# Kernel optimization log

Measured on AMD Instinct MI355X. Metric: run time of the kernel, lower is better.

The kernel has to match this reference:

```python
import jax, jax.numpy as jnp
import numpy as np

DETER, STOCH, ACT, HID, OBS = 1024, 32, 6, 1024, 1024
B, T = 256, 64

def _lin(x, w, b):
    return x @ w.T + b

def setup_inputs() -> dict:
    key = jax.random.key(0)
    ks = iter(jax.random.split(key, 40))
    def p(shape, scale=0.02):
        return (jax.random.normal(next(ks), shape, dtype=jnp.float32) * scale)
    inp = {
        "obs": jax.random.normal(next(ks), (B, T, OBS), dtype=jnp.float32),
        "actions": jax.random.normal(next(ks), (B, T, ACT), dtype=jnp.float32),
        "eps_prior": jax.random.normal(next(ks), (B, T, STOCH), dtype=jnp.float32),
        "eps_post": jax.random.normal(next(ks), (B, T, STOCH), dtype=jnp.float32),
        # input_mlp
        "in_w1": p((HID, STOCH + ACT)), "in_b1": p((HID,)),
        "in_w2": p((HID, HID)), "in_b2": p((HID,)),
        # GRUCell (torch layout: r,z,n chunks)
        "gru_wih": p((3 * DETER, HID)), "gru_whh": p((3 * DETER, DETER)),
        "gru_bih": p((3 * DETER,)), "gru_bhh": p((3 * DETER,)),
        # prior
        "pr_w1": p((HID, DETER)), "pr_b1": p((HID,)),
        "pr_w2": p((HID, HID)), "pr_b2": p((HID,)),
        "pr_mw": p((STOCH, HID)), "pr_mb": p((STOCH,)),
        "pr_sw": p((STOCH, HID)), "pr_sb": p((STOCH,)),
        # posterior
        "po_w1": p((HID, DETER + OBS)), "po_b1": p((HID,)),
        "po_w2": p((HID, HID)), "po_b2": p((HID,)),
        "po_mw": p((STOCH, HID)), "po_mb": p((STOCH,)),
        "po_sw": p((STOCH, HID)), "po_sb": p((STOCH,)),
    }
    return inp

def _rollout(obs, actions, eps_prior, eps_post,
             in_w1, in_b1, in_w2, in_b2,
             gru_wih, gru_whh, gru_bih, gru_bhh,
             pr_w1, pr_b1, pr_w2, pr_b2, pr_mw, pr_mb, pr_sw, pr_sb,
             po_w1, po_b1, po_w2, po_b2, po_mw, po_mb, po_sw, po_sb):
    Bn = obs.shape[0]
    h0 = jnp.zeros((Bn, DETER), obs.dtype)
    z0 = jnp.zeros((Bn, STOCH), obs.dtype)
    a0 = jnp.zeros((Bn, ACT), obs.dtype)

    def step(carry, xs):
        h, z, prev_a = carry
        obs_t, act_t, ep, eq = xs
        x = jnp.concatenate([z, prev_a], axis=-1)
        x = jax.nn.relu(_lin(x, in_w1, in_b1))
        x = jax.nn.relu(_lin(x, in_w2, in_b2))
        # GRUCell
        gi = _lin(x, gru_wih, gru_bih)
        gh = _lin(h, gru_whh, gru_bhh)
        ir, iz, inn = jnp.split(gi, 3, axis=-1)
        hr, hz, hn = jnp.split(gh, 3, axis=-1)
        r = jax.nn.sigmoid(ir + hr)
        u = jax.nn.sigmoid(iz + hz)
        n = jnp.tanh(inn + r * hn)
        h_new = (1.0 - u) * n + u * h
        # prior
        px = jax.nn.relu(_lin(h_new, pr_w1, pr_b1))
        px = jax.nn.relu(_lin(px, pr_w2, pr_b2))
        p_mean = _lin(px, pr_mw, pr_mb)
        p_std = jnp.exp(jnp.clip(_lin(px, pr_sw, pr_sb), -5.0, 2.0))
        # posterior
        qx = jnp.concatenate([h_new, obs_t], axis=-1)
        qx = jax.nn.relu(_lin(qx, po_w1, po_b1))
        qx = jax.nn.relu(_lin(qx, po_w2, po_b2))
        q_mean = _lin(qx, po_mw, po_mb)
        q_std = jnp.exp(jnp.clip(_lin(qx, po_sw, po_sb), -5.0, 2.0))
        z_new = q_mean + q_std * eq
        feat = jnp.concatenate([h_new, z_new], axis=-1)
        return (h_new, z_new, act_t), (feat, p_mean, p_std, q_mean, q_std)

    xs = (jnp.swapaxes(obs, 0, 1), jnp.swapaxes(actions, 0, 1),
          jnp.swapaxes(eps_prior, 0, 1), jnp.swapaxes(eps_post, 0, 1))
    _, (feat, pm, ps, qm, qs) = jax.lax.scan(step, (h0, z0, a0), xs)
    to_bt = lambda a: jnp.swapaxes(a, 0, 1)  # [T,B,...] -> [B,T,...]
    return to_bt(feat), to_bt(pm), to_bt(ps), to_bt(qm), to_bt(qs)

def reference(obs, actions, eps_prior, eps_post,
              in_w1, in_b1, in_w2, in_b2,
              gru_wih, gru_whh, gru_bih, gru_bhh,
              pr_w1, pr_b1, pr_w2, pr_b2, pr_mw, pr_mb, pr_sw, pr_sb,
              po_w1, po_b1, po_w2, po_b2, po_mw, po_mb, po_sw, po_sb):
    return _rollout(obs, actions, eps_prior, eps_post,
                    in_w1, in_b1, in_w2, in_b2,
                    gru_wih, gru_whh, gru_bih, gru_bhh,
                    pr_w1, pr_b1, pr_w2, pr_b2, pr_mw, pr_mb, pr_sw, pr_sb,
                    po_w1, po_b1, po_w2, po_b2, po_mw, po_mb, po_sw, po_sb)
```

## Files before the change

### kernel.cpp

```cpp
#include <hip/hip_runtime.h>
#include <hip/hip_bf16.h>

#define B_   256
#define T_   64
#define OBS_ 1024
#define ACT_ 6
#define STO_ 32
#define HID_ 1024

using bf16 = __bf16;
typedef __attribute__((ext_vector_type(8))) __bf16 bf16x8;
typedef __attribute__((ext_vector_type(4))) float f32x4;

__device__ __forceinline__ f32x4 MF(bf16x8 a, bf16x8 b, f32x4 c) {
  return __builtin_amdgcn_mfma_f32_16x16x32_bf16(a, b, c, 0, 0, 0);
}

struct CvtArgs {
  const float *in_w2, *gru_wih, *gru_whh, *pr_w1, *pr_w2, *po_w1, *po_w2;
  const float *pr_mw, *pr_sw, *po_mw, *po_sw, *obs;
  bf16 *w_in2b, *w_wihb, *w_whhb, *w_pr1b, *w_pr2b, *w_po1hb, *w_po1ob, *w_po2b, *w_headb, *obsb;
};

__global__ void k_cvtall(CvtArgs a) {
  const int row = blockIdx.x;
  const float* src; bf16* dst;
  if      (row < 1024)  { src = a.in_w2   + (size_t)row * 1024;               dst = a.w_in2b  + (size_t)row * 1024; }
  else if (row < 4096)  { int r = row - 1024;  src = a.gru_wih + (size_t)r * 1024;        dst = a.w_wihb  + (size_t)r * 1024; }
  else if (row < 7168)  { int r = row - 4096;  src = a.gru_whh + (size_t)r * 1024;        dst = a.w_whhb  + (size_t)r * 1024; }
  else if (row < 8192)  { int r = row - 7168;  src = a.pr_w1   + (size_t)r * 1024;        dst = a.w_pr1b  + (size_t)r * 1024; }
  else if (row < 9216)  { int r = row - 8192;  src = a.pr_w2   + (size_t)r * 1024;        dst = a.w_pr2b  + (size_t)r * 1024; }
  else if (row < 10240) { int r = row - 9216;  src = a.po_w1   + (size_t)r * 2048;        dst = a.w_po1hb + (size_t)r * 1024; }
  else if (row < 11264) { int r = row - 10240; src = a.po_w1   + (size_t)r * 2048 + 1024; dst = a.w_po1ob + (size_t)r * 1024; }
  else if (row < 12288) { int r = row - 11264; src = a.po_w2   + (size_t)r * 1024;        dst = a.w_po2b  + (size_t)r * 1024; }
  else if (row < 12416) {
    int r = row - 12288;
    const float* hs[4] = { a.pr_mw, a.pr_sw, a.po_mw, a.po_sw };
    src = hs[r >> 5] + (size_t)(r & 31) * 1024;
    dst = a.w_headb + (size_t)r * 1024;
  }
  else { int r = row - 12416; src = a.obs + (size_t)r * 1024; dst = a.obsb + (size_t)r * 1024; }
  const int c = threadIdx.x * 4;
  float4 f = *(const float4*)(src + c);
  dst[c] = (bf16)f.x; dst[c + 1] = (bf16)f.y; dst[c + 2] = (bf16)f.z; dst[c + 3] = (bf16)f.w;
}

__global__ void k_init(const float* __restrict__ in_b1, bf16* __restrict__ x1b,
                       bf16* __restrict__ hbA, bf16* __restrict__ hbB,
                       float* __restrict__ hfA, float* __restrict__ hfB) {
  const int i = blockIdx.x * 256 + threadIdx.x;
  x1b[i] = (bf16)fmaxf(in_b1[i & 1023], 0.f);
  hbA[i] = (bf16)0.f; hbB[i] = (bf16)0.f;
  hfA[i] = 0.f; hfB[i] = 0.f;
}

struct GB2 {
  const bf16 *A1, *A2, *W1, *W2;
  const float* bias;
  bf16* out;
  int lda1, lda2, K1, kseg;
};

__global__ __launch_bounds__(256, 4) void k_l1(GB2 g0, GB2 g1, int s1) {
  GB2 g; int tile;
  if ((int)blockIdx.x < s1) { g = g0; tile = blockIdx.x; }
  else                      { g = g1; tile = blockIdx.x - s1; }
  __shared__ float sh[3 * 1056];
  const int tid = threadIdx.x, lane = tid & 63, kw = tid >> 6;
  const int l15 = lane & 15, kg = lane >> 4, kq = kg * 8, rq = kg * 4;
  const int m0 = (tile & 15) * 16, n0 = (tile >> 4) * 64;
  const int kb = kw * g.kseg;

  const bf16* __restrict__ ap;
  const bf16* __restrict__ wp;
  if (kb < g.K1) {
    ap = g.A1 + (size_t)(m0 + l15) * g.lda1 + kb + kq;
    wp = g.W1 + (size_t)(n0 + l15) * 1024 + kb + kq;
  } else {
    ap = g.A2 + (size_t)(m0 + l15) * g.lda2 + (kb - g.K1) + kq;
    wp = g.W2 + (size_t)(n0 + l15) * 1024 + (kb - g.K1) + kq;
  }
  f32x4 c0{0.f,0.f,0.f,0.f}, c1 = c0, c2 = c0, c3 = c0;
  #pragma unroll 8
  for (int k = 0; k < g.kseg; k += 32) {
    bf16x8 af = *(const bf16x8*)(ap + k);
    c0 = MF(af, *(const bf16x8*)(wp + k            ), c0);
    c1 = MF(af, *(const bf16x8*)(wp + 16 * 1024 + k), c1);
    c2 = MF(af, *(const bf16x8*)(wp + 32 * 1024 + k), c2);
    c3 = MF(af, *(const bf16x8*)(wp + 48 * 1024 + k), c3);
  }
  f32x4 cc[4] = {c0, c1, c2, c3};
  if (kw) {
    float* s = sh + (kw - 1) * 1056;
    #pragma unroll
    for (int t2 = 0; t2 < 4; ++t2)
      #pragma unroll
      for (int r = 0; r < 4; ++r)
        s[(rq + r) * 66 + t2 * 16 + l15] = cc[t2][r];
  }
  __syncthreads();
  if (kw == 0) {
    #pragma unroll
    for (int t2 = 0; t2 < 4; ++t2) {
      const int n = n0 + t2 * 16 + l15;
      const float bv = g.bias[n];
      #pragma unroll
      for (int r = 0; r < 4; ++r) {
        float v = cc[t2][r] + bv;
        #pragma unroll
        for (int s = 0; s < 3; ++s)
          v += sh[s * 1056 + (rq + r) * 66 + t2 * 16 + l15];
        g.out[(size_t)(m0 + rq + r) * 1024 + n] = (bf16)fmaxf(v, 0.f);
      }
    }
  }
}

__global__ __launch_bounds__(512, 2) void k_gru(
    const bf16* __restrict__ hbPrev, const float* __restrict__ hfPrev,
    bf16* __restrict__ hbCur, float* __restrict__ hfCur,
    const bf16* __restrict__ x2b, const bf16* __restrict__ wih,
    const bf16* __restrict__ whh, const float* __restrict__ bih,
    const float* __restrict__ bhh, float* __restrict__ feat, int t) {
  __shared__ float sh[4 * 1088];
  const int mt = blockIdx.x & 3, cs = blockIdx.x >> 2;
  const int tid = threadIdx.x, lane = tid & 63, wv = tid >> 6;
  const int msub = wv & 3, kw = wv >> 2;
  const int l15 = lane & 15, kg = lane >> 4, kq = kg * 8, rq = kg * 4;
  const int mrow = mt * 64 + msub * 16;
  const int c0 = cs * 16;
  const int kb = kw * 512;
  const size_t GOFF = (size_t)1024 * 1024;

  f32x4 ghR{0.f,0.f,0.f,0.f}, ghZ = ghR, ghN = ghR, giR = ghR, giZ = ghR, giN = ghR;
  {
    const bf16* __restrict__ ap = hbPrev + (size_t)(mrow + l15) * 1024 + kb + kq;
    const bf16* __restrict__ wr = whh + (size_t)(c0 + l15) * 1024 + kb + kq;
    #pragma unroll 4
    for (int k = 0; k < 512; k += 32) {
      bf16x8 af = *(const bf16x8*)(ap + k);
      ghR = MF(af, *(const bf16x8*)(wr + k           ), ghR);
      ghZ = MF(af, *(const bf16x8*)(wr + GOFF + k    ), ghZ);
      ghN = MF(af, *(const bf16x8*)(wr + 2 * GOFF + k), ghN);
    }
  }
  {
    const bf16* __restrict__ ap = x2b + (size_t)(mrow + l15) * 1024 + kb + kq;
    const bf16* __restrict__ wr = wih + (size_t)(c0 + l15) * 1024 + kb + kq;
    #pragma unroll 4
    for (int k = 0; k < 512; k += 32) {
      bf16x8 af = *(const bf16x8*)(ap + k);
      giR = MF(af, *(const bf16x8*)(wr + k           ), giR);
      giZ = MF(af, *(const bf16x8*)(wr + GOFF + k    ), giZ);
      giN = MF(af, *(const bf16x8*)(wr + 2 * GOFF + k), giN);
    }
  }
  f32x4 sR = ghR + giR, sZ = ghZ + giZ;
  if (kw) {
    float* s = sh + msub * 1088;
    #pragma unroll
    for (int r = 0; r < 4; ++r) {
      s[      (rq + r) * 17 + l15] = sR[r];
      s[272 + (rq + r) * 17 + l15] = sZ[r];
      s[544 + (rq + r) * 17 + l15] = giN[r];
      s[816 + (rq + r) * 17 + l15] = ghN[r];
    }
  }
  __syncthreads();
  if (kw == 0) {
    const int c = c0 + l15;
    const float bir = bih[c], biz = bih[1024 + c], bin_ = bih[2048 + c];
    const float bhr = bhh[c], bhz = bhh[1024 + c], bhn = bhh[2048 + c];
    const float* s = sh + msub * 1088;
    #pragma unroll
    for (int r = 0; r < 4; ++r) {
      const float vr  = sR[r]  + s[      (rq + r) * 17 + l15];
      const float vz  = sZ[r]  + s[272 + (rq + r) * 17 + l15];
      const float vin = giN[r] + s[544 + (rq + r) * 17 + l15];
      const float vhn = ghN[r] + s[816 + (rq + r) * 17 + l15];
      const int row = mrow + rq + r;
      float rr = vr + bir + bhr;
      float zz = vz + biz + bhz;
      rr = 1.f / (1.f + __expf(-rr));
      zz = 1.f / (1.f + __expf(-zz));
      const float nn = tanhf(vin + bin_ + rr * (vhn + bhn));
      const float h2 = (1.f - zz) * nn + zz * hfPrev[(size_t)row * 1024 + c];
      hbCur[(size_t)row * 1024 + c] = (bf16)h2;
      hfCur[(size_t)row * 1024 + c] = h2;
      feat[((size_t)row * T_ + t) * 1056 + c] = h2;
    }
  }
}

__global__ __launch_bounds__(1024, 1) void k_headfin2(
    const bf16* __restrict__ p2b, const bf16* __restrict__ q2b,
    const bf16* __restrict__ whead,
    const float* __restrict__ pr_mb, const float* __restrict__ pr_sb,
    const float* __restrict__ po_mb, const float* __restrict__ po_sb,
    const float* __restrict__ eps, const float* __restrict__ act,
    const float* __restrict__ in_w1, const float* __restrict__ in_b1,
    float* __restrict__ pm, float* __restrict__ ps,
    float* __restrict__ qm, float* __restrict__ qs,
    float* __restrict__ feat, bf16* __restrict__ x1b, int t) {
  __shared__ float sh[8 * 1056];
  __shared__ float zm[16][32], zs[16][32], zl[16][32], al[16][8];
  const int g = blockIdx.x, m0 = g * 16;
  const int tid = threadIdx.x, lane = tid & 63, w = tid >> 6;
  const int l15 = lane & 15, kg = lane >> 4, kq = kg * 8, rq = kg * 4;

  if (w < 8) {
    const int kw = w & 3, half = w >> 2;
    const bf16* __restrict__ A = half ? q2b : p2b;
    f32x4 c0{0.f,0.f,0.f,0.f}, c1 = c0, c2 = c0, c3 = c0;
    const bf16* __restrict__ ap = A + (size_t)(m0 + l15) * 1024 + kw * 256 + kq;
    const bf16* __restrict__ wp = whead + (size_t)(half * 64 + l15) * 1024 + kw * 256 + kq;
    #pragma unroll
    for (int k = 0; k < 256; k += 32) {
      bf16x8 af = *(const bf16x8*)(ap + k);
      c0 = MF(af, *(const bf16x8*)(wp + k            ), c0);
      c1 = MF(af, *(const bf16x8*)(wp + 16 * 1024 + k), c1);
      c2 = MF(af, *(const bf16x8*)(wp + 32 * 1024 + k), c2);
      c3 = MF(af, *(const bf16x8*)(wp + 48 * 1024 + k), c3);
    }
    f32x4 cc[4] = {c0, c1, c2, c3};
    float* s = sh + w * 1056;
    #pragma unroll
    for (int t2 = 0; t2 < 4; ++t2)
      #pragma unroll
      for (int r = 0; r < 4; ++r)
        s[(rq + r) * 66 + t2 * 16 + l15] = cc[t2][r];
  }
  if (tid >= 928 && tid < 1024) {
    const int idx = tid - 928, r = idx / ACT_, k = idx - r * ACT_;
    al[r][k] = act[((size_t)(m0 + r) * T_ + t) * ACT_ + k];
  }
  __syncthreads();

  #pragma unroll
  for (int rep = 0; rep < 2; ++rep) {
    const int idx = rep * 1024 + tid;
    const int r = idx >> 7, c = idx & 127;
    const int base = (c < 64) ? 0 : 4, cl = c & 63;
    float v = sh[base * 1056 + r * 66 + cl] + sh[(base + 1) * 1056 + r * 66 + cl]
            + sh[(base + 2) * 1056 + r * 66 + cl] + sh[(base + 3) * 1056 + r * 66 + cl];
    const size_t ob = ((size_t)(m0 + r) * T_ + t) * STO_ + (c & 31);
    const int sel = c >> 5;
    if (sel == 0) {
      pm[ob] = v + pr_mb[c];
    } else if (sel == 1) {
      ps[ob] = __expf(fminf(fmaxf(v + pr_sb[c - 32], -5.f), 2.f));
    } else if (sel == 2) {
      const float x = v + po_mb[c - 64];
      qm[ob] = x; zm[r][c - 64] = x;
    } else {
      const float x = __expf(fminf(fmaxf(v + po_sb[c - 96], -5.f), 2.f));
      qs[ob] = x; zs[r][c - 96] = x;
    }
  }
  __syncthreads();
  if (tid < 512) {
    const int r = tid >> 5, j = tid & 31;
    const float z = zm[r][j] + zs[r][j] * eps[((size_t)(m0 + r) * T_ + t) * STO_ + j];
    zl[r][j] = z;
    feat[((size_t)(m0 + r) * T_ + t) * 1056 + 1024 + j] = z;
  }
  __syncthreads();

  const int n = tid;
  float wv_[38];
  #pragma unroll
  for (int j = 0; j < 38; ++j) wv_[j] = in_w1[(size_t)n * 38 + j];
  const float bn = in_b1[n];
  #pragma unroll 2
  for (int r = 0; r < 16; ++r) {
    float a = bn;
    #pragma unroll
    for (int k = 0; k < STO_; ++k) a = fmaf(zl[r][k], wv_[k], a);
    #pragma unroll
    for (int k = 0; k < ACT_; ++k) a = fmaf(al[r][k], wv_[32 + k], a);
    x1b[(size_t)(m0 + r) * 1024 + n] = (bf16)fmaxf(a, 0.f);
  }
}

extern "C" void kernel_launch(void* const* d_in, const int* in_sizes, int n_in,
                              void* d_out, int out_size, void* d_ws, size_t ws_size,
                              hipStream_t stream) {
  (void)in_sizes; (void)n_in; (void)out_size; (void)ws_size;
  const float* obs      = (const float*)d_in[0];
  const float* actions  = (const float*)d_in[1];
  const float* eps_post = (const float*)d_in[3];
  const float* in_w1 = (const float*)d_in[4];
  const float* in_b1 = (const float*)d_in[5];
  const float* in_w2 = (const float*)d_in[6];
  const float* in_b2 = (const float*)d_in[7];
  const float* gru_wih = (const float*)d_in[8];
  const float* gru_whh = (const float*)d_in[9];
  const float* gru_bih = (const float*)d_in[10];
  const float* gru_bhh = (const float*)d_in[11];
  const float* pr_w1 = (const float*)d_in[12];
  const float* pr_b1 = (const float*)d_in[13];
  const float* pr_w2 = (const float*)d_in[14];
  const float* pr_b2 = (const float*)d_in[15];
  const float* pr_mw = (const float*)d_in[16];
  const float* pr_mb = (const float*)d_in[17];
  const float* pr_sw = (const float*)d_in[18];
  const float* pr_sb = (const float*)d_in[19];
  const float* po_w1 = (const float*)d_in[20];
  const float* po_b1 = (const float*)d_in[21];
  const float* po_w2 = (const float*)d_in[22];
  const float* po_b2 = (const float*)d_in[23];
  const float* po_mw = (const float*)d_in[24];
  const float* po_mb = (const float*)d_in[25];
  const float* po_sw = (const float*)d_in[26];
  const float* po_sb = (const float*)d_in[27];

  float* feat = (float*)d_out;
  float* pm = feat + (size_t)B_ * T_ * 1056;
  float* ps = pm + (size_t)B_ * T_ * STO_;
  float* qm = ps + (size_t)B_ * T_ * STO_;
  float* qs = qm + (size_t)B_ * T_ * STO_;

  char* wp_ = (char*)d_ws;
  auto carve = [&](size_t bytes) -> void* {
    void* r = (void*)wp_;
    wp_ += (bytes + 255) & ~(size_t)255;
    return r;
  };
  bf16* w_in2b  = (bf16*)carve((size_t)HID_ * HID_ * 2);
  bf16* w_wihb  = (bf16*)carve((size_t)3 * HID_ * HID_ * 2);
  bf16* w_whhb  = (bf16*)carve((size_t)3 * HID_ * HID_ * 2);
  bf16* w_pr1b  = (bf16*)carve((size_t)HID_ * HID_ * 2);
  bf16* w_pr2b  = (bf16*)carve((size_t)HID_ * HID_ * 2);
  bf16* w_po1hb = (bf16*)carve((size_t)HID_ * HID_ * 2);
  bf16* w_po1ob = (bf16*)carve((size_t)HID_ * OBS_ * 2);
  bf16* w_po2b  = (bf16*)carve((size_t)HID_ * HID_ * 2);
  bf16* w_headb = (bf16*)carve((size_t)128 * HID_ * 2);
  bf16* obsb    = (bf16*)carve((size_t)B_ * T_ * OBS_ * 2);
  bf16* x1b = (bf16*)carve((size_t)B_ * HID_ * 2);
  bf16* x2b = (bf16*)carve((size_t)B_ * HID_ * 2);
  bf16* hbA = (bf16*)carve((size_t)B_ * HID_ * 2);
  bf16* hbB = (bf16*)carve((size_t)B_ * HID_ * 2);
  bf16* p1b = (bf16*)carve((size_t)B_ * HID_ * 2);
  bf16* q1b = (bf16*)carve((size_t)B_ * HID_ * 2);
  bf16* p2b = (bf16*)carve((size_t)B_ * HID_ * 2);
  bf16* q2b = (bf16*)carve((size_t)B_ * HID_ * 2);
  float* hfA = (float*)carve((size_t)B_ * HID_ * 4);
  float* hfB = (float*)carve((size_t)B_ * HID_ * 4);

  CvtArgs ca = { in_w2, gru_wih, gru_whh, pr_w1, pr_w2, po_w1, po_w2,
                 pr_mw, pr_sw, po_mw, po_sw, obs,
                 w_in2b, w_wihb, w_whhb, w_pr1b, w_pr2b, w_po1hb, w_po1ob, w_po2b, w_headb, obsb };
  k_cvtall<<<dim3(28800), dim3(256), 0, stream>>>(ca);
  k_init<<<dim3(1024), dim3(256), 0, stream>>>(in_b1, x1b, hbA, hbB, hfA, hfB);

  GB2 dummy = {};
  for (int t = 0; t < T_; ++t) {
    bf16* hbCur = (t & 1) ? hbB : hbA;
    bf16* hbPrev = (t & 1) ? hbA : hbB;
    float* hfCur = (t & 1) ? hfB : hfA;
    float* hfPrev = (t & 1) ? hfA : hfB;

    GB2 g_x2 = { x1b, nullptr, w_in2b, nullptr, in_b2, x2b, 1024, 0, 1024, 256 };
    k_l1<<<dim3(256), dim3(256), 0, stream>>>(g_x2, dummy, 256);

    k_gru<<<dim3(256), dim3(512), 0, stream>>>(
        hbPrev, hfPrev, hbCur, hfCur, x2b, w_wihb, w_whhb, gru_bih, gru_bhh, feat, t);

    GB2 g_pr1 = { hbCur, nullptr, w_pr1b, nullptr, pr_b1, p1b, 1024, 0, 1024, 256 };
    GB2 g_q1  = { hbCur, obsb + (size_t)t * 1024, w_po1hb, w_po1ob, po_b1, q1b,
                  1024, T_ * 1024, 1024, 512 };
    k_l1<<<dim3(512), dim3(256), 0, stream>>>(g_pr1, g_q1, 256);

    GB2 g_pr2 = { p1b, nullptr, w_pr2b, nullptr, pr_b2, p2b, 1024, 0, 1024, 256 };
    GB2 g_po2 = { q1b, nullptr, w_po2b, nullptr, po_b2, q2b, 1024, 0, 1024, 256 };
    k_l1<<<dim3(512), dim3(256), 0, stream>>>(g_pr2, g_po2, 256);

    k_headfin2<<<dim3(16), dim3(1024), 0, stream>>>(
        p2b, q2b, w_headb, pr_mb, pr_sb, po_mb, po_sb,
        eps_post, actions, in_w1, in_b1, pm, ps, qm, qs, feat, x1b, t);
  }
}
```

Before: 5.791 ms.

## Fuse input MLP second layer into head/finalize kernel via LDS-staged activations

The per-step in_w2 linear layer is folded into the head/finalize kernel. The first-layer activations x1 stay in a swizzled LDS buffer, and an MFMA loop against the bf16 in_w2 produces x2 for the next step. A separate launch is still made once before the loop to seed x2. The grid doubles to 32 blocks, each computing half the output columns; both halves redo the head GEMM, and only one writes the outputs. This removes one kernel launch per step and the global round trip for x1, but the fused GEMM runs on far fewer CUs than the old 256-block launch.

Result: slower. 7.065 ms (+22.0%).

```diff
diff --git a/kernel.cpp b/kernel.cpp
--- a/kernel.cpp
+++ b/kernel.cpp
@@ -192,24 +192,28 @@
   }
 }
 
-__global__ __launch_bounds__(1024, 1) void k_headfin2(
+__global__ __launch_bounds__(1024, 1) void k_fin2(
     const bf16* __restrict__ p2b, const bf16* __restrict__ q2b,
-    const bf16* __restrict__ whead,
+    const bf16* __restrict__ whead, const bf16* __restrict__ win2,
     const float* __restrict__ pr_mb, const float* __restrict__ pr_sb,
     const float* __restrict__ po_mb, const float* __restrict__ po_sb,
+    const float* __restrict__ b_in2,
     const float* __restrict__ eps, const float* __restrict__ act,
     const float* __restrict__ in_w1, const float* __restrict__ in_b1,
     float* __restrict__ pm, float* __restrict__ ps,
     float* __restrict__ qm, float* __restrict__ qs,
-    float* __restrict__ feat, bf16* __restrict__ x1b, int t) {
-  __shared__ float sh[8 * 1056];
-  __shared__ float zm[16][32], zs[16][32], zl[16][32], al[16][8];
-  const int g = blockIdx.x, m0 = g * 16;
-  const int tid = threadIdx.x, lane = tid & 63, w = tid >> 6;
+    float* __restrict__ feat, bf16* __restrict__ x2b, int t) {
+  __shared__ float sh[10112];
+  const int g = blockIdx.x >> 1, nt = blockIdx.x & 1, m0 = g * 16;
+  const int tid = threadIdx.x, lane = tid & 63, wv = tid >> 6;
   const int l15 = lane & 15, kg = lane >> 4, kq = kg * 8, rq = kg * 4;
-
-  if (w < 8) {
-    const int kw = w & 3, half = w >> 2;
+  float* zm = sh + 8448;
+  float* zs = sh + 8960;
+  float* zl = sh + 9472;
+  float* al = sh + 9984;
+
+  if (wv < 8) {
+    const int kw = wv & 3, half = wv >> 2;
     const bf16* __restrict__ A = half ? q2b : p2b;
     f32x4 c0{0.f,0.f,0.f,0.f}, c1 = c0, c2 = c0, c3 = c0;
     const bf16* __restrict__ ap = A + (size_t)(m0 + l15) * 1024 + kw * 256 + kq;
@@ -223,7 +227,7 @@
       c3 = MF(af, *(const bf16x8*)(wp + 48 * 1024 + k), c3);
     }
     f32x4 cc[4] = {c0, c1, c2, c3};
-    float* s = sh + w * 1056;
+    float* s = sh + wv * 1056;
     #pragma unroll
     for (int t2 = 0; t2 < 4; ++t2)
       #pragma unroll
@@ -232,7 +236,7 @@
   }
   if (tid >= 928 && tid < 1024) {
     const int idx = tid - 928, r = idx / ACT_, k = idx - r * ACT_;
-    al[r][k] = act[((size_t)(m0 + r) * T_ + t) * ACT_ + k];
+    al[r * 8 + k] = act[((size_t)(m0 + r) * T_ + t) * ACT_ + k];
   }
   __syncthreads();
 
@@ -240,45 +244,79 @@
   for (int rep = 0; rep < 2; ++rep) {
     const int idx = rep * 1024 + tid;
     const int r = idx >> 7, c = idx & 127;
-    const int base = (c < 64) ? 0 : 4, cl = c & 63;
+    const int base = (c < 64) ? 0 : 4, cl = c & 63, j = c & 31;
     float v = sh[base * 1056 + r * 66 + cl] + sh[(base + 1) * 1056 + r * 66 + cl]
             + sh[(base + 2) * 1056 + r * 66 + cl] + sh[(base + 3) * 1056 + r * 66 + cl];
-    const size_t ob = ((size_t)(m0 + r) * T_ + t) * STO_ + (c & 31);
+    const size_t ob = ((size_t)(m0 + r) * T_ + t) * STO_ + j;
     const int sel = c >> 5;
     if (sel == 0) {
-      pm[ob] = v + pr_mb[c];
+      if (nt == 0) pm[ob] = v + pr_mb[j];
     } else if (sel == 1) {
-      ps[ob] = __expf(fminf(fmaxf(v + pr_sb[c - 32], -5.f), 2.f));
+      if (nt == 0) ps[ob] = __expf(fminf(fmaxf(v + pr_sb[j], -5.f), 2.f));
     } else if (sel == 2) {
-      const float x = v + po_mb[c - 64];
-      qm[ob] = x; zm[r][c - 64] = x;
+      const float x = v + po_mb[j];
+      if (nt == 0) qm[ob] = x;
+      zm[r * 32 + j] = x;
     } else {
-      const float x = __expf(fminf(fmaxf(v + po_sb[c - 96], -5.f), 2.f));
-      qs[ob] = x; zs[r][c - 96] = x;
-    }
-  }
-  __syncthreads();
+      const float x = __expf(fminf(fmaxf(v + po_sb[j], -5.f), 2.f));
+      if (nt == 0) qs[ob] = x;
+      zs[r * 32 + j] = x;
+    }
+  }
+  __syncthreads();
+
   if (tid < 512) {
     const int r = tid >> 5, j = tid & 31;
-    const float z = zm[r][j] + zs[r][j] * eps[((size_t)(m0 + r) * T_ + t) * STO_ + j];
-    zl[r][j] = z;
-    feat[((size_t)(m0 + r) * T_ + t) * 1056 + 1024 + j] = z;
-  }
-  __syncthreads();
-
-  const int n = tid;
-  float wv_[38];
-  #pragma unroll
-  for (int j = 0; j < 38; ++j) wv_[j] = in_w1[(size_t)n * 38 + j];
-  const float bn = in_b1[n];
-  #pragma unroll 2
-  for (int r = 0; r < 16; ++r) {
-    float a = bn;
-    #pragma unroll
-    for (int k = 0; k < STO_; ++k) a = fmaf(zl[r][k], wv_[k], a);
-    #pragma unroll
-    for (int k = 0; k < ACT_; ++k) a = fmaf(al[r][k], wv_[32 + k], a);
-    x1b[(size_t)(m0 + r) * 1024 + n] = (bf16)fmaxf(a, 0.f);
+    const float z = zm[r * 32 + j] + zs[r * 32 + j] * eps[((size_t)(m0 + r) * T_ + t) * STO_ + j];
+    zl[r * 32 + j] = z;
+    if (nt == 0) feat[((size_t)(m0 + r) * T_ + t) * 1056 + 1024 + j] = z;
+  }
+  __syncthreads();
+
+  {
+    char* x1c = (char*)sh;
+    const int n = tid;
+    const float* w = in_w1 + (size_t)n * 38;
+    float wreg[38];
+    #pragma unroll
+    for (int j = 0; j < 38; ++j) wreg[j] = w[j];
+    const float bn = in_b1[n];
+    const int chunk = n >> 3, sub = (n & 7) * 2;
+    #pragma unroll 2
+    for (int r = 0; r < 16; ++r) {
+      float a = bn;
+      #pragma unroll
+      for (int k = 0; k < STO_; ++k) a = fmaf(zl[r * 32 + k], wreg[k], a);
+      #pragma unroll
+      for (int k = 0; k < ACT_; ++k) a = fmaf(al[r * 8 + k], wreg[32 + k], a);
+      *(bf16*)(x1c + r * 2048 + ((chunk ^ (r & 7)) << 4) + sub) = (bf16)fmaxf(a, 0.f);
+    }
+  }
+  __syncthreads();
+
+  {
+    const char* x1c = (const char*)sh;
+    const int colbase = nt * 512 + wv * 32;
+    f32x4 e0{0.f,0.f,0.f,0.f}, e1 = e0;
+    const bf16* __restrict__ wp = win2 + (size_t)(colbase + l15) * 1024 + kq;
+    #pragma unroll 4
+    for (int k = 0; k < 1024; k += 32) {
+      const int chunk = (k + kq) >> 3;
+      bf16x8 af = *(const bf16x8*)(x1c + l15 * 2048 + ((chunk ^ (l15 & 7)) << 4));
+      e0 = MF(af, *(const bf16x8*)(wp + k            ), e0);
+      e1 = MF(af, *(const bf16x8*)(wp + 16 * 1024 + k), e1);
+    }
+    f32x4 ee[2] = {e0, e1};
+    #pragma unroll
+    for (int nf = 0; nf < 2; ++nf) {
+      const int col = colbase + nf * 16 + l15;
+      const float bv = b_in2[col];
+      #pragma unroll
+      for (int r = 0; r < 4; ++r) {
+        const int row = m0 + rq + r;
+        x2b[(size_t)row * 1024 + col] = (bf16)fmaxf(ee[nf][r] + bv, 0.f);
+      }
+    }
   }
 }
 
@@ -354,15 +392,15 @@
   k_init<<<dim3(1024), dim3(256), 0, stream>>>(in_b1, x1b, hbA, hbB, hfA, hfB);
 
   GB2 dummy = {};
+  GB2 g_x2i = { x1b, nullptr, w_in2b, nullptr, in_b2, x2b, 1024, 0, 1024, 256 };
+  k_l1<<<dim3(256), dim3(256), 0, stream>>>(g_x2i, dummy, 256);
+
   for (int t = 0; t < T_; ++t) {
     bf16* hbCur = (t & 1) ? hbB : hbA;
     bf16* hbPrev = (t & 1) ? hbA : hbB;
     float* hfCur = (t & 1) ? hfB : hfA;
     float* hfPrev = (t & 1) ? hfA : hfB;
 
-    GB2 g_x2 = { x1b, nullptr, w_in2b, nullptr, in_b2, x2b, 1024, 0, 1024, 256 };
-    k_l1<<<dim3(256), dim3(256), 0, stream>>>(g_x2, dummy, 256);
-
     k_gru<<<dim3(256), dim3(512), 0, stream>>>(
         hbPrev, hfPrev, hbCur, hfCur, x2b, w_wihb, w_whhb, gru_bih, gru_bhh, feat, t);
 
@@ -375,8 +413,8 @@
     GB2 g_po2 = { q1b, nullptr, w_po2b, nullptr, po_b2, q2b, 1024, 0, 1024, 256 };
     k_l1<<<dim3(512), dim3(256), 0, stream>>>(g_pr2, g_po2, 256);
 
-    k_headfin2<<<dim3(16), dim3(1024), 0, stream>>>(
-        p2b, q2b, w_headb, pr_mb, pr_sb, po_mb, po_sb,
-        eps_post, actions, in_w1, in_b1, pm, ps, qm, qs, feat, x1b, t);
-  }
-}
+    k_fin2<<<dim3(32), dim3(1024), 0, stream>>>(
+        p2b, q2b, w_headb, w_in2b, pr_mb, pr_sb, po_mb, po_sb, in_b2,
+        eps_post, actions, in_w1, in_b1, pm, ps, qm, qs, feat, x2b, t);
+  }
+}
```
